# Kernel optimization log

Measured on AMD Instinct MI355X. Metric: run time of the kernel, lower is better.

## Reference

```python
import jax, jax.numpy as jnp
import numpy as np

L = 512  # lstm/hidden size
A = 1000  # num_actions
D = 512  # input size


def setup_inputs() -> dict:
    key = jax.random.key(0)
    ks = jax.random.split(key, 20)
    TB = 65536
    B = 256
    def lin(k, out_d, in_d):
        k1, k2 = jax.random.split(k)
        W = jax.random.normal(k1, (out_d, in_d), jnp.float32) / np.sqrt(in_d)
        b = jnp.zeros((out_d,), jnp.float32)
        return W, b
    W_t1, b_t1 = lin(ks[0], L, D)
    W_t2, b_t2 = lin(ks[1], L, L)
    Wih = jax.random.normal(ks[2], (4 * L, L), jnp.float32) / np.sqrt(L)
    Whh = jax.random.normal(ks[3], (4 * L, L), jnp.float32) / np.sqrt(L)
    bih = jnp.zeros((4 * L,), jnp.float32)
    bhh = jnp.zeros((4 * L,), jnp.float32)
    Wa1, ba1 = lin(ks[4], L, L)
    Wa2, ba2 = lin(ks[5], A, L)
    Wa2 = Wa2 * 0.01
    Wc1, bc1 = lin(ks[6], L, L)
    Wc2, bc2 = lin(ks[7], 1, L)
    h0 = jax.random.normal(ks[8], (B, L), jnp.float32)
    c0 = jax.random.normal(ks[9], (B, L), jnp.float32)
    x = jax.random.normal(ks[10], (TB, D), jnp.float32)
    done = jax.random.randint(ks[11], (TB,), 0, 2, jnp.int32)
    action = jax.random.randint(ks[12], (TB,), 0, A, jnp.int32)
    return {
        "x": x, "done": done, "action": action, "B": B,
        "W_t1": W_t1, "b_t1": b_t1, "W_t2": W_t2, "b_t2": b_t2,
        "Wih": Wih, "Whh": Whh, "bih": bih, "bhh": bhh,
        "Wa1": Wa1, "ba1": ba1, "Wa2": Wa2, "ba2": ba2,
        "Wc1": Wc1, "bc1": bc1, "Wc2": Wc2, "bc2": bc2,
        "h0": h0, "c0": c0,
    }


def reference(x, done, action, B, W_t1, b_t1, W_t2, b_t2, Wih, Whh, bih, bhh,
              Wa1, ba1, Wa2, ba2, Wc1, bc1, Wc2, bc2, h0, c0):
    # trunk: tanh MLP
    h = jnp.tanh(x @ W_t1.T + b_t1)
    h = jnp.tanh(h @ W_t2.T + b_t2)  # (T*B, L)
    T = h.shape[0] // B
    hs = h.reshape(T, B, L)
    ds = done.reshape(T, B).astype(jnp.float32)

    def step(carry, inp):
        hp, cp = carry
        xt, dt = inp
        m = (1.0 - dt)[:, None]  # reset state where done
        hp = hp * m
        cp = cp * m
        gates = xt @ Wih.T + bih + hp @ Whh.T + bhh  # (B, 4L)
        i, f, g, o = jnp.split(gates, 4, axis=-1)  # PyTorch gate order i,f,g,o
        c = jax.nn.sigmoid(f) * cp + jax.nn.sigmoid(i) * jnp.tanh(g)
        hn = jax.nn.sigmoid(o) * jnp.tanh(c)
        return (hn, c), hn

    (_, _), outs = jax.lax.scan(step, (h0, c0), (hs, ds))
    new_hidden = outs.reshape(T * B, L) + h  # residual LSTM

    # actor head
    a = jnp.tanh(new_hidden @ Wa1.T + ba1)
    logits = a @ Wa2.T + ba2  # (T*B, A)
    logp_all = jax.nn.log_softmax(logits, axis=-1)
    lp = jnp.take_along_axis(logp_all, action[:, None].astype(jnp.int32), axis=1)[:, 0]
    ent = -jnp.sum(jnp.exp(logp_all) * logp_all, axis=-1)

    # critic head
    ch = jnp.tanh(new_hidden @ Wc1.T + bc1)
    v = (ch @ Wc2.T + bc2)[:, 0]

    return jnp.stack([lp, ent, v])  # (3, T*B)
```

## Files before the change

### kernel.cpp

```cpp
#include <hip/hip_runtime.h>
#include <hip/hip_bf16.h>

typedef short v8s __attribute__((ext_vector_type(8)));
typedef float v4f __attribute__((ext_vector_type(4)));

#define S0R 12
#define NLEV 244
#define L2E 1.4426950408889634f

__device__ __forceinline__ float bf2f(unsigned short u) {
    union { unsigned int i; float f; } v; v.i = ((unsigned int)u) << 16; return v.f;
}
__device__ __forceinline__ unsigned short f2bf(float f) {
    union { float f; unsigned int i; } v; v.f = f;
    unsigned int x = v.i;
    return (unsigned short)((x + 0x7fffu + ((x >> 16) & 1u)) >> 16);
}
__device__ __forceinline__ float fsig(float x) {
    return __builtin_amdgcn_rcpf(1.f + __builtin_amdgcn_exp2f(-L2E * x));
}
__device__ __forceinline__ float ftanh(float x) {
    return 2.f * __builtin_amdgcn_rcpf(1.f + __builtin_amdgcn_exp2f((-2.f * L2E) * x)) - 1.f;
}

__device__ __forceinline__ void gld_lds16(const unsigned short* g, unsigned short* l) {
    __builtin_amdgcn_global_load_lds(
        (const __attribute__((address_space(1))) unsigned int*)g,
        (__attribute__((address_space(3))) unsigned int*)l, 16, 0, 0);
}

template <bool TANH>
__global__ __launch_bounds__(512, 2)
void gemm256(const unsigned short* __restrict__ Ag, const unsigned short* __restrict__ Wg,
             const float* __restrict__ b1,
             unsigned short* __restrict__ Cg, int Nreal, int Npad, int Ntiles, int Astr)
{
    __shared__ __align__(16) unsigned short As[2][256 * 64];
    __shared__ __align__(16) unsigned short Bs[2][256 * 64];

    const int tid  = threadIdx.x;
    const int w    = tid >> 6;
    const int lane = tid & 63;
    const int quad = lane >> 4;
    const int lr   = lane & 15;
    const int wm   = w >> 2;
    const int wn   = w & 3;

    const int nwg = gridDim.x;
    const int cpx = nwg >> 3;
    const int swz = (blockIdx.x & 7) * cpx + (blockIdx.x >> 3);
    const int m0  = (swz / Ntiles) * 256;
    const int n0  = (swz % Ntiles) * 256;

    const unsigned short* gA = Ag + (size_t)m0 * Astr;
    const unsigned short* gB = Wg + (size_t)n0 * 512;

    const int sr  = w * 8 + (lane >> 3);
    const int skg = (lane & 7) ^ ((lane >> 3) & 7);

    auto SA = [&](int buf, int u, int kt) {
        gld_lds16(gA + (size_t)(u * 64 + sr) * Astr + kt * 64 + skg * 8,
                  &As[buf][(u * 64 + w * 8) * 64]);
    };
    auto SB = [&](int buf, int u, int kt) {
        gld_lds16(gB + (size_t)(u * 64 + sr) * 512 + kt * 64 + skg * 8,
                  &Bs[buf][(u * 64 + w * 8) * 64]);
    };

    const int g8_0  = (quad ^ (lr & 7)) * 8;
    const int g8_1  = ((quad + 4) ^ (lr & 7)) * 8;
    const int aBase = (wm * 128 + lr) * 64;
    const int bBase = (wn * 64 + lr) * 64;

    v4f zz = {0.f, 0.f, 0.f, 0.f};
    v4f acc[8][4];
    #pragma unroll
    for (int m = 0; m < 8; ++m)
        #pragma unroll
        for (int n = 0; n < 4; ++n) acc[m][n] = zz;
    v8s Bf[4][2];

#define DSB(BUF)                                                         \
    _Pragma("unroll")                                                    \
    for (int n = 0; n < 4; ++n) {                                        \
        Bf[n][0] = *(const v8s*)&Bs[BUF][bBase + n * 1024 + g8_0];       \
        Bf[n][1] = *(const v8s*)&Bs[BUF][bBase + n * 1024 + g8_1];       \
    }

#define PH(BUF, Q, STMTS, PREBAR)                                                     \
    {                                                                                 \
        const v8s a00 = *(const v8s*)&As[BUF][aBase + ((Q)*2 + 0) * 1024 + g8_0];     \
        const v8s a01 = *(const v8s*)&As[BUF][aBase + ((Q)*2 + 0) * 1024 + g8_1];     \
        const v8s a10 = *(const v8s*)&As[BUF][aBase + ((Q)*2 + 1) * 1024 + g8_0];     \
        const v8s a11 = *(const v8s*)&As[BUF][aBase + ((Q)*2 + 1) * 1024 + g8_1];     \
        STMTS;                                                                        \
        PREBAR;                                                                       \
        __builtin_amdgcn_s_barrier();                                                 \
        asm volatile("s_waitcnt lgkmcnt(0)" ::: "memory");                            \
        __builtin_amdgcn_sched_barrier(0);                                            \
        __builtin_amdgcn_s_setprio(1);                                                \
        _Pragma("unroll")                                                             \
        for (int n = 0; n < 4; ++n) {                                                 \
            acc[(Q)*2    ][n] = __builtin_amdgcn_mfma_f32_16x16x32_bf16(a00, Bf[n][0], acc[(Q)*2    ][n], 0, 0, 0); \
            acc[(Q)*2    ][n] = __builtin_amdgcn_mfma_f32_16x16x32_bf16(a01, Bf[n][1], acc[(Q)*2    ][n], 0, 0, 0); \
            acc[(Q)*2 + 1][n] = __builtin_amdgcn_mfma_f32_16x16x32_bf16(a10, Bf[n][0], acc[(Q)*2 + 1][n], 0, 0, 0); \
            acc[(Q)*2 + 1][n] = __builtin_amdgcn_mfma_f32_16x16x32_bf16(a11, Bf[n][1], acc[(Q)*2 + 1][n], 0, 0, 0); \
        }                                                                             \
        __builtin_amdgcn_s_setprio(0);                                                \
        __builtin_amdgcn_s_barrier();                                                 \
    }

    SB(0, 0, 0); SB(0, 1, 0); SB(0, 2, 0); SB(0, 3, 0);
    SA(0, 0, 0); SA(0, 2, 0); SA(0, 1, 0); SA(0, 3, 0);
    SB(1, 0, 1); SB(1, 1, 1); SB(1, 2, 1); SB(1, 3, 1);
    SA(1, 0, 1); SA(1, 2, 1);
    asm volatile("s_waitcnt vmcnt(6)" ::: "memory");
    __builtin_amdgcn_s_barrier();

    #pragma unroll
    for (int i = 0; i < 4; ++i) {
        const bool more = (i < 3);
        const int t1 = 2 * i + 1, t2 = 2 * i + 2, t3 = 2 * i + 3;
        PH(0, 0, { DSB(0); SA(1, 1, t1); SA(1, 3, t1); }, )
        PH(0, 1, { if (more) { SB(0, 0, t2); SB(0, 1, t2); } }, )
        PH(0, 2, { if (more) { SB(0, 2, t2); SB(0, 3, t2); } }, )
        PH(0, 3, { if (more) { SA(0, 0, t2); SA(0, 2, t2); } },
           if (more) { asm volatile("s_waitcnt vmcnt(6)" ::: "memory"); }
           else      { asm volatile("s_waitcnt vmcnt(0)" ::: "memory"); } )
        PH(1, 0, { DSB(1); if (more) { SA(0, 1, t2); SA(0, 3, t2); } }, )
        PH(1, 1, { if (more) { SB(1, 0, t3); SB(1, 1, t3); } }, )
        PH(1, 2, { if (more) { SB(1, 2, t3); SB(1, 3, t3); } }, )
        PH(1, 3, { if (more) { SA(1, 0, t3); SA(1, 2, t3); } },
           if (more) { asm volatile("s_waitcnt vmcnt(6)" ::: "memory"); } )
    }
#undef PH
#undef DSB

    __syncthreads();
    unsigned short* Ct = wm ? &Bs[0][0] : &As[0][0];
    #pragma unroll
    for (int n = 0; n < 4; ++n) {
        const int nn = n0 + wn * 64 + n * 16 + lr;
        const float bias = (nn < Nreal) ? b1[nn] : 0.f;
        const int col = wn * 64 + n * 16 + lr;
        #pragma unroll
        for (int m = 0; m < 8; ++m) {
            #pragma unroll
            for (int r = 0; r < 4; ++r) {
                const int row = m * 16 + quad * 4 + r;
                float v = acc[m][n][r] + bias;
                if (TANH) v = ftanh(v);
                Ct[row * 256 + (((col >> 3) ^ (row & 7)) << 3) + (col & 7)] = f2bf(v);
            }
        }
    }
    __syncthreads();
    #pragma unroll
    for (int it = 0; it < 16; ++it) {
        const int c   = it * 512 + tid;
        const int row = c >> 5;
        const int gc  = c & 31;
        const unsigned short* src = (row < 128)
            ? &As[0][row * 256 + ((gc ^ (row & 7)) << 3)]
            : &Bs[0][(row - 128) * 256 + ((gc ^ (row & 7)) << 3)];
        v8s val = *(const v8s*)src;
        *(v8s*)&Cg[(size_t)(m0 + row) * Npad + n0 + gc * 8] = val;
    }
}

__global__ void cvt8(const float* __restrict__ src, unsigned short* __restrict__ dst)
{
    const size_t i = ((size_t)blockIdx.x * 256 + threadIdx.x) * 8;
    float4 f0 = *(const float4*)(src + i);
    float4 f1 = *(const float4*)(src + i + 4);
    unsigned short t8[8];
    t8[0]=f2bf(f0.x); t8[1]=f2bf(f0.y); t8[2]=f2bf(f0.z); t8[3]=f2bf(f0.w);
    t8[4]=f2bf(f1.x); t8[5]=f2bf(f1.y); t8[6]=f2bf(f1.z); t8[7]=f2bf(f1.w);
    *(v8s*)(dst + i) = *(const v8s*)t8;
}

__global__ void cvt_cat(const float* __restrict__ Whh, const float* __restrict__ Wih,
                        unsigned short* __restrict__ Wcat)
{
    const size_t i = ((size_t)blockIdx.x * 256 + threadIdx.x) * 8;
    const int row = (int)(i >> 10), col = (int)(i & 1023);
    const float* src = (col < 512) ? &Whh[(size_t)row * 512 + col]
                                   : &Wih[(size_t)row * 512 + (col - 512)];
    float4 f0 = *(const float4*)src;
    float4 f1 = *(const float4*)(src + 4);
    unsigned short t8[8];
    t8[0]=f2bf(f0.x); t8[1]=f2bf(f0.y); t8[2]=f2bf(f0.z); t8[3]=f2bf(f0.w);
    t8[4]=f2bf(f1.x); t8[5]=f2bf(f1.y); t8[6]=f2bf(f1.z); t8[7]=f2bf(f1.w);
    *(v8s*)(Wcat + i) = *(const v8s*)t8;
}

__global__ void wa2pad(const float* __restrict__ src, unsigned short* __restrict__ dst)
{
    const int i = blockIdx.x * 256 + threadIdx.x;
    const int row = i >> 9;
    dst[i] = (row < 1000) ? f2bf(src[(size_t)row * 512 + (i & 511)]) : (unsigned short)0;
}

__global__ void prep_misc(const float* __restrict__ bih, const float* __restrict__ bhh,
                          const float* __restrict__ ba1, const float* __restrict__ bc1,
                          float* __restrict__ bsum, float* __restrict__ bac)
{
    const int i = blockIdx.x * 256 + threadIdx.x;
    if (i < 2048) bsum[i] = bih[i] + bhh[i];
    else if (i < 3072) {
        int k = i - 2048;
        bac[k] = (k < 512) ? ba1[k] : bc1[k - 512];
    }
}

__global__ void init_state(const float* __restrict__ h0, const float* __restrict__ c0,
                           const int* __restrict__ done,
                           unsigned short* __restrict__ h_init, unsigned short* __restrict__ c_init,
                           unsigned short* __restrict__ zbuf)
{
    const int b = blockIdx.x;
    const float m = 1.f - (float)done[b];
    for (int k = threadIdx.x; k < 512; k += 256) {
        h_init[(size_t)b * 512 + k] = f2bf(h0[(size_t)b * 512 + k] * m);
        c_init[(size_t)b * 512 + k] = f2bf(c0[(size_t)b * 512 + k] * m);
        if (b == 0) zbuf[k] = 0;
    }
}

__global__ __launch_bounds__(256, 1)
void seg_prep(const int* __restrict__ done, int* __restrict__ rows,
              int* __restrict__ counts, int* __restrict__ offs,
              int* __restrict__ trows, int* __restrict__ tcnt, int* __restrict__ toffs,
              int* __restrict__ maxS, int* __restrict__ bar, int T)
{
    __shared__ unsigned int   bits[256][8];
    __shared__ unsigned short cnt[256][S0R];
    __shared__ unsigned short base[256][S0R];
    __shared__ int tot[S0R];
    __shared__ int goff[S0R];
    __shared__ int tcl[NLEV];
    __shared__ int tol[NLEV];
    __shared__ int tpos[NLEV];
    __shared__ int mxl[256];
    const int b = threadIdx.x;
    #pragma unroll
    for (int s = 0; s < S0R; ++s) cnt[b][s] = 0;
    #pragma unroll
    for (int i = 0; i < 8; ++i) bits[b][i] = 0;
    for (int l = b; l < NLEV; l += 256) { tcl[l] = 0; tpos[l] = 0; }
    __syncthreads();

    int s = 0, mx = 0;
    for (int t0 = 0; t0 < T; t0 += 8) {
        int d8[8];
        #pragma unroll
        for (int i = 0; i < 8; ++i) d8[i] = done[(t0 + i) * 256 + b];
        #pragma unroll
        for (int i = 0; i < 8; ++i) {
            const int t = t0 + i, d = d8[i];
            if (d) bits[b][t >> 5] |= (1u << (t & 31));
            s = (t == 0 || d) ? 0 : s + 1;
            if (s < S0R) { if (t != 0) cnt[b][s]++; }
            else atomicAdd(&tcl[s - S0R], 1);
            mx = mx > s ? mx : s;
        }
    }
    mxl[b] = mx;
    __syncthreads();

    if (b < S0R) {
        int tsum = 0;
        for (int bb = 0; bb < 256; ++bb) { base[bb][b] = (unsigned short)tsum; tsum += cnt[bb][b]; }
        tot[b] = tsum;
    }
    __syncthreads();
    if (b == 0) {
        int run = 256;
        for (int ss = 0; ss < S0R; ++ss) { goff[ss] = run; run += tot[ss]; }
        run = 0;
        for (int l = 0; l < NLEV; ++l) { tol[l] = run; run += tcl[l]; }
        int m = 0;
        for (int bb = 0; bb < 256; ++bb) m = m > mxl[bb] ? m : mxl[bb];
        *maxS = m;
        *bar  = 0;
    }
    __syncthreads();
    if (b < S0R) {
        counts[b] = tot[b] + (b == 0 ? 256 : 0);
        offs[b]   = (b == 0) ? 0 : goff[b];
    }
    for (int l = b; l < NLEV; l += 256) { tcnt[l] = tcl[l]; toffs[l] = tol[l]; }

    s = 0;
    for (int t = 0; t < T; ++t) {
        int d = (bits[b][t >> 5] >> (t & 31)) & 1;
        s = (t == 0 || d) ? 0 : s + 1;
        if (t == 0) {
            rows[b] = b;
        } else if (s < S0R) {
            int idx = goff[s] + (int)base[b][s];
            base[b][s]++;
            rows[idx] = t * 256 + b;
        } else {
            int idx = tol[s - S0R] + atomicAdd(&tpos[s - S0R], 1);
            trows[idx] = t * 256 + b;
        }
    }
}

__global__ __launch_bounds__(256, 4)
void lstm_round(const int* __restrict__ rows, const int* __restrict__ counts,
                const int* __restrict__ offs, int s,
                const unsigned short* __restrict__ H2,
                const unsigned short* __restrict__ Wcat,
                const float* __restrict__ bsum,
                const unsigned short* __restrict__ h_init,
                const unsigned short* __restrict__ c_init,
                const unsigned short* __restrict__ zbuf,
                unsigned short* __restrict__ Hraw, unsigned short* __restrict__ Cst,
                unsigned short* __restrict__ Hnew)
{
    const int M = counts[s];
    if (M == 0) return;
    const int off    = offs[s];
    const int mtiles = (M + 127) >> 7;

    __shared__ __align__(16) unsigned short U[17408];
    __shared__ float bls[128];
    __shared__ int rl[128];
    unsigned short* const Gx = U;

    const int tid  = threadIdx.x;
    const int w    = tid >> 6;
    const int lane = tid & 63;
    const int quad = lane >> 4;
    const int lr   = lane & 15;
    const int wm   = w & 1, wn = w >> 1;
    const int srow = lane >> 2;
    const int kblk = (lane & 3) ^ ((lane >> 3) & 3);

    const int nrt = gridDim.x >> 4;
    const int bid = blockIdx.x;
    int r0, c0i;
    if (nrt >= 4) {
        const int xcd = bid & 7, j = bid >> 3;
        r0  = (xcd >> 1) + ((j >> 3) << 2);
        c0i = ((xcd & 1) << 3) + (j & 7);
    } else {
        r0  = bid % nrt;
        c0i = bid / nrt;
    }
    const int c0 = c0i * 32;

    if (tid < 128) bls[tid] = bsum[(tid >> 5) * 512 + c0 + (tid & 31)];

    const int br0 = w * 16 + srow;
    const int br1 = 64 + br0;
    const unsigned short* gB0 = Wcat + (size_t)((br0 >> 5) * 512 + c0 + (br0 & 31)) * 1024 + kblk * 8;
    const unsigned short* gB1 = Wcat + (size_t)((br1 >> 5) * 512 + c0 + (br1 & 31)) * 1024 + kblk * 8;

    const int swz = (quad ^ ((lr >> 1) & 3)) * 8;
    int aoff[4], boff[4];
    #pragma unroll
    for (int i = 0; i < 4; ++i) {
        aoff[i] = (wm * 64 + i * 16 + lr) * 32 + swz;
        boff[i] = (wn * 64 + i * 16 + lr) * 32 + swz;
    }

    for (int mt = r0; mt < mtiles; mt += nrt) {
        __syncthreads();
        if (tid < 128) {
            int li = mt * 128 + tid;
            rl[tid] = (li < M) ? rows[off + li] : -1;
        }
        __syncthreads();

        const int kbeg = (s == 0 && mt * 128 >= 256) ? 16 : 0;

        int g0r = rl[w * 16 + srow];
        int g1r = rl[64 + w * 16 + srow];
        const unsigned short* gA0h;
        const unsigned short* gA1h;
        if (s == 0) {
            gA0h = (g0r >= 0 && g0r < 256) ? h_init + (size_t)g0r * 512 + kblk * 8 : zbuf + kblk * 8;
            gA1h = (g1r >= 0 && g1r < 256) ? h_init + (size_t)g1r * 512 + kblk * 8 : zbuf + kblk * 8;
        } else {
            gA0h = (g0r >= 0) ? Hraw + (size_t)(g0r - 256) * 512 + kblk * 8 : zbuf + kblk * 8;
            gA1h = (g1r >= 0) ? Hraw + (size_t)(g1r - 256) * 512 + kblk * 8 : zbuf + kblk * 8;
        }
        const unsigned short* gA0x = (g0r >= 0) ? H2 + (size_t)g0r * 512 + kblk * 8 : zbuf + kblk * 8;
        const unsigned short* gA1x = (g1r >= 0) ? H2 + (size_t)g1r * 512 + kblk * 8 : zbuf + kblk * 8;

        auto STG = [&](int b, int k) {
            const unsigned short* a0 = (k < 16) ? gA0h + k * 32 : gA0x + (k - 16) * 32;
            const unsigned short* a1 = (k < 16) ? gA1h + k * 32 : gA1x + (k - 16) * 32;
            unsigned short* base = U + b * 8192;
            gld_lds16(a0, base + (w * 16) * 32);
            gld_lds16(a1, base + (64 + w * 16) * 32);
            gld_lds16(gB0 + k * 32, base + 4096 + (w * 16) * 32);
            gld_lds16(gB1 + k * 32, base + 4096 + (64 + w * 16) * 32);
        };

        v4f zz = {0.f, 0.f, 0.f, 0.f};
        v4f acc[4][4] = {{zz,zz,zz,zz},{zz,zz,zz,zz},{zz,zz,zz,zz},{zz,zz,zz,zz}};

        STG(0, kbeg);
        #pragma unroll 2
        for (int k = kbeg; k < 32; ++k) {
            if (k < 31) {
                STG((k + 1) & 1, k + 1);
                asm volatile("s_waitcnt vmcnt(4)" ::: "memory");
            } else {
                asm volatile("s_waitcnt vmcnt(0)" ::: "memory");
            }
            __builtin_amdgcn_s_barrier();
            __builtin_amdgcn_sched_barrier(0);
            const unsigned short* Ab = U + (k & 1) * 8192;
            const unsigned short* Bb = Ab + 4096;
            v8s a[4], b[4];
            #pragma unroll
            for (int i = 0; i < 4; ++i) { a[i] = *(const v8s*)&Ab[aoff[i]]; b[i] = *(const v8s*)&Bb[boff[i]]; }
            __builtin_amdgcn_s_setprio(1);
            #pragma unroll
            for (int i = 0; i < 4; ++i)
                #pragma unroll
                for (int j = 0; j < 4; ++j)
                    acc[i][j] = __builtin_amdgcn_mfma_f32_16x16x32_bf16(a[i], b[j], acc[i][j], 0, 0, 0);
            __builtin_amdgcn_s_setprio(0);
            __builtin_amdgcn_s_barrier();
            __builtin_amdgcn_sched_barrier(0);
        }

        #pragma unroll
        for (int j = 0; j < 4; ++j) {
            const int nl = wn * 64 + j * 16 + lr;
            #pragma unroll
            for (int i = 0; i < 4; ++i)
                #pragma unroll
                for (int r = 0; r < 4; ++r)
                    Gx[(wm * 64 + i * 16 + quad * 4 + r) * 136 + nl] = f2bf(acc[i][j][r]);
        }
        __syncthreads();

        {
            const int rloc = tid >> 1;
            const int half = tid & 1;
            const int gr   = rl[rloc];
            if (gr >= 0) {
                #pragma unroll
                for (int ch = 0; ch < 2; ++ch) {
                    const int co = half * 16 + ch * 8;
                    const int kg = c0 + co;
                    v8s q0 = *(const v8s*)&Gx[rloc * 136 +   0 + co];
                    v8s q1 = *(const v8s*)&Gx[rloc * 136 +  32 + co];
                    v8s q2 = *(const v8s*)&Gx[rloc * 136 +  64 + co];
                    v8s q3 = *(const v8s*)&Gx[rloc * 136 +  96 + co];
                    v8s h2v = *(const v8s*)&H2[(size_t)gr * 512 + kg];
                    float cprev[8];
                    if (s == 0) {
                        if (gr < 256) {
                            v8s cv = *(const v8s*)&c_init[(size_t)gr * 512 + kg];
                            #pragma unroll
                            for (int e = 0; e < 8; ++e) cprev[e] = bf2f((unsigned short)cv[e]);
                        } else {
                            #pragma unroll
                            for (int e = 0; e < 8; ++e) cprev[e] = 0.f;
                        }
                    } else {
                        v8s cv = *(const v8s*)&Cst[(size_t)(gr - 256) * 512 + kg];
                        #pragma unroll
                        for (int e = 0; e < 8; ++e) cprev[e] = bf2f((unsigned short)cv[e]);
                    }
                    unsigned short hc[8], cc[8], hn[8];
                    #pragma unroll
                    for (int e = 0; e < 8; ++e) {
                        float gi = bf2f((unsigned short)q0[e]) + bls[ 0 + co + e];
                        float gf = bf2f((unsigned short)q1[e]) + bls[32 + co + e];
                        float gg = bf2f((unsigned short)q2[e]) + bls[64 + co + e];
                        float go = bf2f((unsigned short)q3[e]) + bls[96 + co + e];
                        float c  = fsig(gf) * cprev[e] + fsig(gi) * ftanh(gg);
                        float h  = fsig(go) * ftanh(c);
                        cc[e] = f2bf(c);
                        hc[e] = f2bf(h);
                        hn[e] = f2bf(h + bf2f((unsigned short)h2v[e]));
                    }
                    *(v8s*)&Cst[(size_t)gr * 512 + kg]  = *(const v8s*)cc;
                    *(v8s*)&Hraw[(size_t)gr * 512 + kg] = *(const v8s*)hc;
                    *(v8s*)&Hnew[(size_t)gr * 512 + kg] = *(const v8s*)hn;
                }
            }
        }
    }
}

__global__ __launch_bounds__(256, 1)
void lstm_tail(const int* __restrict__ trows, const int* __restrict__ tcnt,
               const int* __restrict__ toffs, const int* __restrict__ maxS_p,
               const unsigned short* __restrict__ H2,
               const unsigned short* __restrict__ Wcat,
               const float* __restrict__ bsum,
               unsigned short* __restrict__ Hraw, unsigned short* __restrict__ Cst,
               unsigned short* __restrict__ Hnew,
               int* __restrict__ bar)
{
    const int mS = *maxS_p;
    if (mS < S0R) return;
    __shared__ __align__(16) unsigned short Wl[32 * 1024];
    __shared__ __align__(16) unsigned short Hb[16 * 1024];
    __shared__ float Gb[16 * 32];
    __shared__ float bl[32];
    __shared__ int rl[16];
    const int j    = blockIdx.x;
    const int tid  = threadIdx.x;
    const int w    = tid >> 6;
    const int lane = tid & 63;
    const int quad = lane >> 4;
    const int lr   = lane & 15;

    if (tid < 32) bl[tid] = bsum[(tid >> 3) * 512 + j * 8 + (tid & 7)];

    for (int e = tid; e < 32 * 128; e += 256) {
        int n = e >> 7, kb = e & 127;
        int g = n >> 3, c = n & 7;
        *(v8s*)&Wl[n * 1024 + kb * 8] = *(const v8s*)&Wcat[(size_t)(g * 512 + j * 8 + c) * 1024 + kb * 8];
    }

    int target = 0;
    for (int s = S0R; s <= mS; ++s) {
        const int lev = s - S0R;
        const int M   = tcnt[lev];
        const int off = toffs[lev];
        for (int ch = 0; ch < M; ch += 16) {
            __syncthreads();
            if (tid < 16) rl[tid] = (ch + tid < M) ? trows[off + ch + tid] : -1;
            __syncthreads();
            {
                int r = tid >> 4, seg = (tid & 15) * 32;
                int gr = rl[r];
                if (gr >= 0) {
                    const unsigned short* srcH = &Hraw[(size_t)(gr - 256) * 512 + seg];
                    const unsigned short* srcX = &H2[(size_t)gr * 512 + seg];
                    #pragma unroll
                    for (int q = 0; q < 4; ++q) {
                        *(v8s*)&Hb[r * 1024 + seg + q * 8]       = *(const v8s*)(srcH + q * 8);
                        *(v8s*)&Hb[r * 1024 + 512 + seg + q * 8] = *(const v8s*)(srcX + q * 8);
                    }
                } else {
                    v8s z = {0,0,0,0,0,0,0,0};
                    #pragma unroll
                    for (int q = 0; q < 4; ++q) {
                        *(v8s*)&Hb[r * 1024 + seg + q * 8]       = z;
                        *(v8s*)&Hb[r * 1024 + 512 + seg + q * 8] = z;
                    }
                }
            }
            __syncthreads();
            if (w < 2) {
                v4f acc = {0.f, 0.f, 0.f, 0.f};
                for (int k = 0; k < 32; ++k) {
                    v8s a = *(const v8s*)&Hb[lr * 1024 + k * 32 + quad * 8];
                    v8s b = *(const v8s*)&Wl[(w * 16 + lr) * 1024 + k * 32 + quad * 8];
                    acc = __builtin_amdgcn_mfma_f32_16x16x32_bf16(a, b, acc, 0, 0, 0);
                }
                #pragma unroll
                for (int r = 0; r < 4; ++r)
                    Gb[(quad * 4 + r) * 32 + w * 16 + lr] = acc[r];
            }
            __syncthreads();
            if (tid < 128) {
                int r = tid >> 3, c = tid & 7;
                int gr = rl[r];
                if (gr >= 0) {
                    int k = j * 8 + c;
                    float gi = Gb[r * 32 +  0 + c] + bl[ 0 + c];
                    float gf = Gb[r * 32 +  8 + c] + bl[ 8 + c];
                    float gg = Gb[r * 32 + 16 + c] + bl[16 + c];
                    float go = Gb[r * 32 + 24 + c] + bl[24 + c];
                    float cp = bf2f(Cst[(size_t)(gr - 256) * 512 + k]);
                    float cc = fsig(gf) * cp + fsig(gi) * ftanh(gg);
                    float hh = fsig(go) * ftanh(cc);
                    Cst[(size_t)gr * 512 + k]  = f2bf(cc);
                    Hraw[(size_t)gr * 512 + k] = f2bf(hh);
                    Hnew[(size_t)gr * 512 + k] = f2bf(hh + bf2f(H2[(size_t)gr * 512 + k]));
                }
            }
        }
        target += 64;
        __threadfence();
        __syncthreads();
        if (tid == 0) {
            __hip_atomic_fetch_add(bar, 1, __ATOMIC_RELEASE, __HIP_MEMORY_SCOPE_AGENT);
            while (__hip_atomic_load(bar, __ATOMIC_ACQUIRE, __HIP_MEMORY_SCOPE_AGENT) < target) {}
        }
        __syncthreads();
        __threadfence();
    }
}

__global__ void head_reduce(const unsigned short* __restrict__ logits,
                            const int* __restrict__ action,
                            float* __restrict__ out, int TB)
{
    const int r = blockIdx.x * 4 + (threadIdx.x >> 6);
    const int lane = threadIdx.x & 63;
    const unsigned short* row = logits + (size_t)r * 1024;
    float m = -1e30f, Z = 0.f, S = 0.f;
    v8s v0 = *(const v8s*)&row[lane * 8];
    #pragma unroll
    for (int e = 0; e < 8; ++e) {
        float xv = bf2f((unsigned short)v0[e]);
        if (xv > m) { float sc = __builtin_amdgcn_exp2f((m - xv) * L2E); Z *= sc; S *= sc; m = xv; }
        float ev = __builtin_amdgcn_exp2f((xv - m) * L2E);
        Z += ev; S += xv * ev;
    }
    v8s v1 = *(const v8s*)&row[512 + lane * 8];
    #pragma unroll
    for (int e = 0; e < 8; ++e) {
        int c = 512 + lane * 8 + e;
        if (c < 1000) {
            float xv = bf2f((unsigned short)v1[e]);
            if (xv > m) { float sc = __builtin_amdgcn_exp2f((m - xv) * L2E); Z *= sc; S *= sc; m = xv; }
            float ev = __builtin_amdgcn_exp2f((xv - m) * L2E);
            Z += ev; S += xv * ev;
        }
    }
    #pragma unroll
    for (int offb = 32; offb > 0; offb >>= 1) {
        float m2 = __shfl_xor(m, offb);
        float Z2 = __shfl_xor(Z, offb);
        float S2 = __shfl_xor(S, offb);
        float M  = fmaxf(m, m2);
        float s1 = __builtin_amdgcn_exp2f((m - M) * L2E), s2 = __builtin_amdgcn_exp2f((m2 - M) * L2E);
        Z = Z * s1 + Z2 * s2;
        S = S * s1 + S2 * s2;
        m = M;
    }
    if (lane == 0) {
        float lse = m + 0.6931471805599453f * __builtin_amdgcn_logf(Z);
        float xa  = bf2f(row[action[r]]);
        out[r]      = xa - lse;
        out[TB + r] = lse - S / Z;
    }
}

__global__ void critic_v(const unsigned short* __restrict__ AC, const float* __restrict__ Wc2,
                         const float* __restrict__ bc2, float* __restrict__ out, int TB)
{
    const int r = blockIdx.x * 4 + (threadIdx.x >> 6);
    const int lane = threadIdx.x & 63;
    const unsigned short* row = AC + (size_t)r * 1024 + 512;
    v8s hv = *(const v8s*)&row[lane * 8];
    float4 w0 = *(const float4*)&Wc2[lane * 8];
    float4 w1 = *(const float4*)&Wc2[lane * 8 + 4];
    float s = bf2f((unsigned short)hv[0]) * w0.x + bf2f((unsigned short)hv[1]) * w0.y +
              bf2f((unsigned short)hv[2]) * w0.z + bf2f((unsigned short)hv[3]) * w0.w +
              bf2f((unsigned short)hv[4]) * w1.x + bf2f((unsigned short)hv[5]) * w1.y +
              bf2f((unsigned short)hv[6]) * w1.z + bf2f((unsigned short)hv[7]) * w1.w;
    #pragma unroll
    for (int offb = 32; offb > 0; offb >>= 1) s += __shfl_xor(s, offb);
    if (lane == 0) out[2 * TB + r] = s + bc2[0];
}

extern "C" void kernel_launch(void* const* d_in, const int* in_sizes, int n_in,
                              void* d_out, int out_size, void* d_ws, size_t ws_size,
                              hipStream_t stream)
{
    const float* x    = (const float*)d_in[0];
    const int*  done  = (const int*)d_in[1];
    const int*  action= (const int*)d_in[2];
    const float* W_t1 = (const float*)d_in[4];
    const float* b_t1 = (const float*)d_in[5];
    const float* W_t2 = (const float*)d_in[6];
    const float* b_t2 = (const float*)d_in[7];
    const float* Wih  = (const float*)d_in[8];
    const float* Whh  = (const float*)d_in[9];
    const float* bih  = (const float*)d_in[10];
    const float* bhh  = (const float*)d_in[11];
    const float* Wa1  = (const float*)d_in[12];
    const float* ba1  = (const float*)d_in[13];
    const float* Wa2  = (const float*)d_in[14];
    const float* ba2  = (const float*)d_in[15];
    const float* Wc1  = (const float*)d_in[16];
    const float* bc1  = (const float*)d_in[17];
    const float* Wc2  = (const float*)d_in[18];
    const float* bc2  = (const float*)d_in[19];
    const float* h0   = (const float*)d_in[20];
    const float* c0   = (const float*)d_in[21];
    float* out = (float*)d_out;

    const int TB = in_sizes[1];
    const int T  = TB / 256;

    const size_t MiB = 1024 * 1024;
    char* ws = (char*)d_ws;
    unsigned short* H1     = (unsigned short*)(ws);
    unsigned short* Hnew   = (unsigned short*)(ws);
    unsigned short* logits = (unsigned short*)(ws);
    unsigned short* AC1    = (unsigned short*)(ws + 128 * MiB);
    unsigned short* Cst    = (unsigned short*)(ws + 256 * MiB);
    unsigned short* H2     = (unsigned short*)(ws + 320 * MiB);
    unsigned short* Hraw   = (unsigned short*)(ws + 384 * MiB);
    unsigned short* xbf    = Hraw;
    unsigned short* Wt1b   = (unsigned short*)(ws + 448 * MiB);
    unsigned short* Wt2b   = Wt1b + 512 * 512;
    unsigned short* Wcat   = Wt2b + 512 * 512;
    unsigned short* Wacb   = Wcat + 2048 * 1024;
    unsigned short* Wa2b   = Wacb + 1024 * 512;
    unsigned short* h_init = Wa2b + 1024 * 512;
    unsigned short* c_init = h_init + 256 * 512;
    unsigned short* zbuf   = c_init + 256 * 512;
    int* rows   = (int*)(zbuf + 512);
    int* trows  = rows + 65536;
    int* counts = trows + 65536;
    int* offs   = counts + S0R;
    int* tcnt   = offs + S0R;
    int* toffs  = tcnt + NLEV;
    int* maxS   = toffs + NLEV;
    int* bar    = maxS + 1;
    float* bsum = (float*)(bar + 1);
    float* bac  = bsum + 2048;

    dim3 blk(256);
    dim3 blk5(512);

    cvt8<<<16384, blk, 0, stream>>>(x, xbf);
    cvt8<<<128,  blk, 0, stream>>>(W_t1, Wt1b);
    cvt8<<<128,  blk, 0, stream>>>(W_t2, Wt2b);
    cvt_cat<<<1024, blk, 0, stream>>>(Whh, Wih, Wcat);
    cvt8<<<128,  blk, 0, stream>>>(Wa1, Wacb);
    cvt8<<<128,  blk, 0, stream>>>(Wc1, Wacb + 512 * 512);
    wa2pad<<<2048, blk, 0, stream>>>(Wa2, Wa2b);
    prep_misc<<<12, blk, 0, stream>>>(bih, bhh, ba1, bc1, bsum, bac);
    init_state<<<256, blk, 0, stream>>>(h0, c0, done, h_init, c_init, zbuf);
    seg_prep<<<1, blk, 0, stream>>>(done, rows, counts, offs, trows, tcnt, toffs, maxS, bar, T);

    gemm256<true ><<<512, blk5, 0, stream>>>(xbf, Wt1b, b_t1, H1, 512, 512, 2, 512);
    gemm256<true ><<<512, blk5, 0, stream>>>(H1,  Wt2b, b_t2, H2, 512, 512, 2, 512);

    static const int Gs[S0R] = {256, 128, 64, 32, 16, 8, 4, 2, 1, 1, 1, 1};
    for (int s = 0; s < S0R; ++s)
        lstm_round<<<dim3(16 * Gs[s]), blk, 0, stream>>>(rows, counts, offs, s, H2, Wcat, bsum,
                                                         h_init, c_init, zbuf, Hraw, Cst, Hnew);
    lstm_tail<<<64, blk, 0, stream>>>(trows, tcnt, toffs, maxS, H2, Wcat, bsum, Hraw, Cst, Hnew, bar);

    gemm256<true ><<<1024, blk5, 0, stream>>>(Hnew, Wacb, bac, AC1, 1024, 1024, 4, 512);

    gemm256<false><<<1024, blk5, 0, stream>>>(AC1, Wa2b, ba2, logits, 1000, 1024, 4, 1024);
    head_reduce<<<TB / 4, blk, 0, stream>>>(logits, action, out, TB);

    critic_v<<<TB / 4, blk, 0, stream>>>(AC1, Wc2, bc2, out, TB);
}
```

Baseline: 1.263 ms.

## Fuse x fp32→bf16 conversion into first GEMM and softmax partials into logits GEMM

Replaces the separate conversion pass over x with a new 128x128-tile GEMM that loads fp32 activations, converts them to bf16 in registers and stages them into LDS, so the bf16 copy of x is no longer written and reread. The logits GEMM now computes per-row partial max, sum-exp, sum x·exp and the action logit for its 256-column tile straight from LDS and writes a float4 per tile. A small combine kernel merges the partials, which removes the full bf16 logits write and its reread by the old reduction. The reduction inside the GEMM epilogue is serial across 32 rows per wave and may lengthen the epilogue.

```diff
diff --git a/kernel.cpp b/kernel.cpp
--- a/kernel.cpp
+++ b/kernel.cpp
@@ -29,11 +29,12 @@
         (__attribute__((address_space(3))) unsigned int*)l, 16, 0, 0);
 }
 
-template <bool TANH>
+template <bool TANH, bool REDUCE>
 __global__ __launch_bounds__(512, 2)
 void gemm256(const unsigned short* __restrict__ Ag, const unsigned short* __restrict__ Wg,
              const float* __restrict__ b1,
-             unsigned short* __restrict__ Cg, int Nreal, int Npad, int Ntiles, int Astr)
+             unsigned short* __restrict__ Cg, int Nreal, int Npad, int Ntiles, int Astr,
+             const int* __restrict__ act, float4* __restrict__ P)
 {
     __shared__ __align__(16) unsigned short As[2][256 * 64];
     __shared__ __align__(16) unsigned short Bs[2][256 * 64];
@@ -155,16 +156,187 @@
         }
     }
     __syncthreads();
-    #pragma unroll
-    for (int it = 0; it < 16; ++it) {
-        const int c   = it * 512 + tid;
-        const int row = c >> 5;
-        const int gc  = c & 31;
-        const unsigned short* src = (row < 128)
-            ? &As[0][row * 256 + ((gc ^ (row & 7)) << 3)]
-            : &Bs[0][(row - 128) * 256 + ((gc ^ (row & 7)) << 3)];
-        v8s val = *(const v8s*)src;
-        *(v8s*)&Cg[(size_t)(m0 + row) * Npad + n0 + gc * 8] = val;
+
+    if (!REDUCE) {
+        #pragma unroll
+        for (int it = 0; it < 16; ++it) {
+            const int c   = it * 512 + tid;
+            const int row = c >> 5;
+            const int gc  = c & 31;
+            const unsigned short* src = (row < 128)
+                ? &As[0][row * 256 + ((gc ^ (row & 7)) << 3)]
+                : &Bs[0][(row - 128) * 256 + ((gc ^ (row & 7)) << 3)];
+            v8s val = *(const v8s*)src;
+            *(v8s*)&Cg[(size_t)(m0 + row) * Npad + n0 + gc * 8] = val;
+        }
+    } else {
+        const int wr0 = w * 32;
+        for (int rr = 0; rr < 32; ++rr) {
+            const int row = wr0 + rr;
+            const unsigned short* src = (row < 128) ? &As[0][row * 256]
+                                                    : &Bs[0][(row - 128) * 256];
+            const int rk = row & 7;
+            float xv[4];
+            float m = -3.0e38f;
+            #pragma unroll
+            for (int e = 0; e < 4; ++e) {
+                const int col = lane * 4 + e;
+                xv[e] = (n0 + col < Nreal)
+                      ? bf2f(src[(((col >> 3) ^ rk) << 3) + (col & 7)]) : -3.0e38f;
+                m = fmaxf(m, xv[e]);
+            }
+            float Z = 0.f, S = 0.f;
+            #pragma unroll
+            for (int e = 0; e < 4; ++e) {
+                if (n0 + lane * 4 + e < Nreal) {
+                    float ev = __builtin_amdgcn_exp2f((xv[e] - m) * L2E);
+                    Z += ev; S += xv[e] * ev;
+                }
+            }
+            #pragma unroll
+            for (int ob = 32; ob > 0; ob >>= 1) {
+                float m2 = __shfl_xor(m, ob), Z2 = __shfl_xor(Z, ob), S2 = __shfl_xor(S, ob);
+                float M2 = fmaxf(m, m2);
+                float s1 = __builtin_amdgcn_exp2f((m - M2) * L2E);
+                float s2 = __builtin_amdgcn_exp2f((m2 - M2) * L2E);
+                Z = Z * s1 + Z2 * s2; S = S * s1 + S2 * s2; m = M2;
+            }
+            if (lane == 0) {
+                const int grow = m0 + row;
+                const int ac   = act[grow] - n0;
+                float xa = -3.0e38f;
+                if (ac >= 0 && ac < 256)
+                    xa = bf2f(src[(((ac >> 3) ^ rk) << 3) + (ac & 7)]);
+                P[(size_t)grow * 4 + (n0 >> 8)] = make_float4(m, Z, S, xa);
+            }
+        }
+    }
+}
+
+__global__ void head_combine(const float4* __restrict__ P, float* __restrict__ out, int TB)
+{
+    const int r = blockIdx.x * 256 + threadIdx.x;
+    float4 p0 = P[(size_t)r * 4 + 0], p1 = P[(size_t)r * 4 + 1];
+    float4 p2 = P[(size_t)r * 4 + 2], p3 = P[(size_t)r * 4 + 3];
+    float M = fmaxf(fmaxf(p0.x, p1.x), fmaxf(p2.x, p3.x));
+    float s0 = __builtin_amdgcn_exp2f((p0.x - M) * L2E);
+    float s1 = __builtin_amdgcn_exp2f((p1.x - M) * L2E);
+    float s2 = __builtin_amdgcn_exp2f((p2.x - M) * L2E);
+    float s3 = __builtin_amdgcn_exp2f((p3.x - M) * L2E);
+    float Z = p0.y * s0 + p1.y * s1 + p2.y * s2 + p3.y * s3;
+    float S = p0.z * s0 + p1.z * s1 + p2.z * s2 + p3.z * s3;
+    float xa = fmaxf(fmaxf(p0.w, p1.w), fmaxf(p2.w, p3.w));
+    float lse = M + 0.6931471805599453f * __builtin_amdgcn_logf(Z);
+    out[r]      = xa - lse;
+    out[TB + r] = lse - S / Z;
+}
+
+__global__ __launch_bounds__(256, 3)
+void gemm128cvt(const float* __restrict__ Ag, const unsigned short* __restrict__ Wg,
+                const float* __restrict__ b1, unsigned short* __restrict__ Cg)
+{
+    __shared__ __align__(16) unsigned short SS[2][8192];
+
+    const int tid  = threadIdx.x;
+    const int w    = tid >> 6;
+    const int lane = tid & 63;
+    const int quad = lane >> 4;
+    const int lr   = lane & 15;
+    const int wm   = w & 1, wn = w >> 1;
+    const int srow = lane >> 2;
+    const int kblk = (lane & 3) ^ ((lane >> 3) & 3);
+
+    const int cpx = gridDim.x >> 3;
+    const int swz = (blockIdx.x & 7) * cpx + (blockIdx.x >> 3);
+    const int mt = swz >> 2, nt = swz & 3;
+
+    const float* gA0 = Ag + (size_t)(mt * 128 + w * 16 + srow) * 512 + kblk * 8;
+    const float* gA1 = gA0 + (size_t)64 * 512;
+    const unsigned short* gB0 = Wg + (size_t)(nt * 128 + w * 16 + srow) * 512 + kblk * 8;
+    const unsigned short* gB1 = gB0 + (size_t)64 * 512;
+
+    const int swl = (quad ^ ((lr >> 1) & 3)) * 8;
+    int aoff[4], boff[4];
+    #pragma unroll
+    for (int i = 0; i < 4; ++i) {
+        aoff[i] = (wm * 64 + i * 16 + lr) * 32 + swl;
+        boff[i] = (wn * 64 + i * 16 + lr) * 32 + swl;
+    }
+    const int adst = (w * 16 + srow) * 32 + (lane & 3) * 8;
+
+    v4f zz = {0.f, 0.f, 0.f, 0.f};
+    v4f acc[4][4] = {{zz,zz,zz,zz},{zz,zz,zz,zz},{zz,zz,zz,zz},{zz,zz,zz,zz}};
+
+    float4 aw[2][4];
+    aw[0][0] = *(const float4*)(gA0);
+    aw[0][1] = *(const float4*)(gA0 + 4);
+    aw[0][2] = *(const float4*)(gA1);
+    aw[0][3] = *(const float4*)(gA1 + 4);
+    gld_lds16(gB0, &SS[0][4096 + (w * 16) * 32]);
+    gld_lds16(gB1, &SS[0][4096 + (64 + w * 16) * 32]);
+
+    #pragma unroll 2
+    for (int k = 0; k < 16; ++k) {
+        const int cur = k & 1, nxt = cur ^ 1;
+        if (k < 15) {
+            aw[nxt][0] = *(const float4*)(gA0 + (k + 1) * 32);
+            aw[nxt][1] = *(const float4*)(gA0 + (k + 1) * 32 + 4);
+            aw[nxt][2] = *(const float4*)(gA1 + (k + 1) * 32);
+            aw[nxt][3] = *(const float4*)(gA1 + (k + 1) * 32 + 4);
+            gld_lds16(gB0 + (k + 1) * 32, &SS[nxt][4096 + (w * 16) * 32]);
+            gld_lds16(gB1 + (k + 1) * 32, &SS[nxt][4096 + (64 + w * 16) * 32]);
+        }
+        unsigned short t0[8], t1[8];
+        t0[0]=f2bf(aw[cur][0].x); t0[1]=f2bf(aw[cur][0].y); t0[2]=f2bf(aw[cur][0].z); t0[3]=f2bf(aw[cur][0].w);
+        t0[4]=f2bf(aw[cur][1].x); t0[5]=f2bf(aw[cur][1].y); t0[6]=f2bf(aw[cur][1].z); t0[7]=f2bf(aw[cur][1].w);
+        t1[0]=f2bf(aw[cur][2].x); t1[1]=f2bf(aw[cur][2].y); t1[2]=f2bf(aw[cur][2].z); t1[3]=f2bf(aw[cur][2].w);
+        t1[4]=f2bf(aw[cur][3].x); t1[5]=f2bf(aw[cur][3].y); t1[6]=f2bf(aw[cur][3].z); t1[7]=f2bf(aw[cur][3].w);
+        *(v8s*)&SS[cur][adst]        = *(const v8s*)t0;
+        *(v8s*)&SS[cur][adst + 2048] = *(const v8s*)t1;
+        if (k < 15) asm volatile("s_waitcnt vmcnt(6)" ::: "memory");
+        else        asm volatile("s_waitcnt vmcnt(0)" ::: "memory");
+        asm volatile("s_waitcnt lgkmcnt(0)" ::: "memory");
+        __builtin_amdgcn_s_barrier();
+        __builtin_amdgcn_sched_barrier(0);
+        const unsigned short* Ab = &SS[cur][0];
+        const unsigned short* Bb = &SS[cur][4096];
+        v8s a[4], b[4];
+        #pragma unroll
+        for (int i = 0; i < 4; ++i) { a[i] = *(const v8s*)&Ab[aoff[i]]; b[i] = *(const v8s*)&Bb[boff[i]]; }
+        __builtin_amdgcn_s_setprio(1);
+        #pragma unroll
+        for (int i = 0; i < 4; ++i)
+            #pragma unroll
+            for (int j = 0; j < 4; ++j)
+                acc[i][j] = __builtin_amdgcn_mfma_f32_16x16x32_bf16(a[i], b[j], acc[i][j], 0, 0, 0);
+        __builtin_amdgcn_s_setprio(0);
+        __builtin_amdgcn_s_barrier();
+        __builtin_amdgcn_sched_barrier(0);
+    }
+
+    __syncthreads();
+    unsigned short* Ct = &SS[0][0];
+    #pragma unroll
+    for (int j = 0; j < 4; ++j) {
+        const int col = wn * 64 + j * 16 + lr;
+        const float bias = b1[nt * 128 + col];
+        #pragma unroll
+        for (int i = 0; i < 4; ++i) {
+            #pragma unroll
+            for (int r = 0; r < 4; ++r) {
+                const int row = wm * 64 + i * 16 + quad * 4 + r;
+                Ct[row * 128 + (((col >> 3) ^ (row & 15)) << 3) + (col & 7)] =
+                    f2bf(ftanh(acc[i][j][r] + bias));
+            }
+        }
+    }
+    __syncthreads();
+    #pragma unroll
+    for (int it = 0; it < 8; ++it) {
+        const int idx = it * 256 + tid;
+        const int row = idx >> 4, g = idx & 15;
+        v8s val = *(const v8s*)&Ct[row * 128 + ((g ^ (row & 15)) << 3)];
+        *(v8s*)&Cg[(size_t)(mt * 128 + row) * 512 + nt * 128 + g * 8] = val;
     }
 }
 
@@ -597,52 +769,6 @@
     }
 }
 
-__global__ void head_reduce(const unsigned short* __restrict__ logits,
-                            const int* __restrict__ action,
-                            float* __restrict__ out, int TB)
-{
-    const int r = blockIdx.x * 4 + (threadIdx.x >> 6);
-    const int lane = threadIdx.x & 63;
-    const unsigned short* row = logits + (size_t)r * 1024;
-    float m = -1e30f, Z = 0.f, S = 0.f;
-    v8s v0 = *(const v8s*)&row[lane * 8];
-    #pragma unroll
-    for (int e = 0; e < 8; ++e) {
-        float xv = bf2f((unsigned short)v0[e]);
-        if (xv > m) { float sc = __builtin_amdgcn_exp2f((m - xv) * L2E); Z *= sc; S *= sc; m = xv; }
-        float ev = __builtin_amdgcn_exp2f((xv - m) * L2E);
-        Z += ev; S += xv * ev;
-    }
-    v8s v1 = *(const v8s*)&row[512 + lane * 8];
-    #pragma unroll
-    for (int e = 0; e < 8; ++e) {
-        int c = 512 + lane * 8 + e;
-        if (c < 1000) {
-            float xv = bf2f((unsigned short)v1[e]);
-            if (xv > m) { float sc = __builtin_amdgcn_exp2f((m - xv) * L2E); Z *= sc; S *= sc; m = xv; }
-            float ev = __builtin_amdgcn_exp2f((xv - m) * L2E);
-            Z += ev; S += xv * ev;
-        }
-    }
-    #pragma unroll
-    for (int offb = 32; offb > 0; offb >>= 1) {
-        float m2 = __shfl_xor(m, offb);
-        float Z2 = __shfl_xor(Z, offb);
-        float S2 = __shfl_xor(S, offb);
-        float M  = fmaxf(m, m2);
-        float s1 = __builtin_amdgcn_exp2f((m - M) * L2E), s2 = __builtin_amdgcn_exp2f((m2 - M) * L2E);
-        Z = Z * s1 + Z2 * s2;
-        S = S * s1 + S2 * s2;
-        m = M;
-    }
-    if (lane == 0) {
-        float lse = m + 0.6931471805599453f * __builtin_amdgcn_logf(Z);
-        float xa  = bf2f(row[action[r]]);
-        out[r]      = xa - lse;
-        out[TB + r] = lse - S / Z;
-    }
-}
-
 __global__ void critic_v(const unsigned short* __restrict__ AC, const float* __restrict__ Wc2,
                          const float* __restrict__ bc2, float* __restrict__ out, int TB)
 {
@@ -695,12 +821,11 @@
     char* ws = (char*)d_ws;
     unsigned short* H1     = (unsigned short*)(ws);
     unsigned short* Hnew   = (unsigned short*)(ws);
-    unsigned short* logits = (unsigned short*)(ws);
+    float4*         P      = (float4*)(ws);
     unsigned short* AC1    = (unsigned short*)(ws + 128 * MiB);
     unsigned short* Cst    = (unsigned short*)(ws + 256 * MiB);
     unsigned short* H2     = (unsigned short*)(ws + 320 * MiB);
     unsigned short* Hraw   = (unsigned short*)(ws + 384 * MiB);
-    unsigned short* xbf    = Hraw;
     unsigned short* Wt1b   = (unsigned short*)(ws + 448 * MiB);
     unsigned short* Wt2b   = Wt1b + 512 * 512;
     unsigned short* Wcat   = Wt2b + 512 * 512;
@@ -723,7 +848,6 @@
     dim3 blk(256);
     dim3 blk5(512);
 
-    cvt8<<<16384, blk, 0, stream>>>(x, xbf);
     cvt8<<<128,  blk, 0, stream>>>(W_t1, Wt1b);
     cvt8<<<128,  blk, 0, stream>>>(W_t2, Wt2b);
     cvt_cat<<<1024, blk, 0, stream>>>(Whh, Wih, Wcat);
@@ -734,8 +858,9 @@
     init_state<<<256, blk, 0, stream>>>(h0, c0, done, h_init, c_init, zbuf);
     seg_prep<<<1, blk, 0, stream>>>(done, rows, counts, offs, trows, tcnt, toffs, maxS, bar, T);
 
-    gemm256<true ><<<512, blk5, 0, stream>>>(xbf, Wt1b, b_t1, H1, 512, 512, 2, 512);
-    gemm256<true ><<<512, blk5, 0, stream>>>(H1,  Wt2b, b_t2, H2, 512, 512, 2, 512);
+    gemm128cvt<<<2048, blk, 0, stream>>>(x, Wt1b, b_t1, H1);
+    gemm256<true, false><<<512, blk5, 0, stream>>>(H1, Wt2b, b_t2, H2, 512, 512, 2, 512,
+                                                   nullptr, nullptr);
 
     static const int Gs[S0R] = {256, 128, 64, 32, 16, 8, 4, 2, 1, 1, 1, 1};
     for (int s = 0; s < S0R; ++s)
@@ -743,10 +868,12 @@
                                                          h_init, c_init, zbuf, Hraw, Cst, Hnew);
     lstm_tail<<<64, blk, 0, stream>>>(trows, tcnt, toffs, maxS, H2, Wcat, bsum, Hraw, Cst, Hnew, bar);
 
-    gemm256<true ><<<1024, blk5, 0, stream>>>(Hnew, Wacb, bac, AC1, 1024, 1024, 4, 512);
-
-    gemm256<false><<<1024, blk5, 0, stream>>>(AC1, Wa2b, ba2, logits, 1000, 1024, 4, 1024);
-    head_reduce<<<TB / 4, blk, 0, stream>>>(logits, action, out, TB);
+    gemm256<true, false><<<1024, blk5, 0, stream>>>(Hnew, Wacb, bac, AC1, 1024, 1024, 4, 512,
+                                                    nullptr, nullptr);
+
+    gemm256<false, true><<<1024, blk5, 0, stream>>>(AC1, Wa2b, ba2, nullptr, 1000, 1024, 4, 1024,
+                                                    action, P);
+    head_combine<<<TB / 256, blk, 0, stream>>>(P, out, TB);
 
     critic_v<<<TB / 4, blk, 0, stream>>>(AC1, Wc2, bc2, out, TB);
 }
```

Result: slower. 1.315 ms (+4.2%).
